# Kernel optimization log

Hardware: AMD Instinct MI355X
Metric: run time of the kernel (lower is better)

Reference implementation:

```python
import jax, jax.numpy as jnp
import numpy as np

M_POS = 0.5
M_NEG_SIM = 0.1
LAM_NEG = 1.0


def setup_inputs() -> dict:
    key = jax.random.key(0)
    N, d, G = 8192, 1024, 64
    codebook = jax.random.normal(key, (N, d), dtype=jnp.float32)
    base = (jnp.arange(N) // G) * G  # contiguous groups of size G (vq_to_range)
    starts = base.astype(jnp.int32)
    ends = (base + G - 1).astype(jnp.int32)
    return {"codebook": codebook, "starts": starts, "ends": ends, "max_i": N - 1}


def reference(codebook, starts, ends, max_i):
    N, d = codebook.shape
    M = min(N, int(max_i) + 1)  # rows processed by the python loop

    # cosine similarity rows [0:M] vs all N
    zn = codebook / jnp.linalg.norm(codebook, axis=-1, keepdims=True)
    cos = jnp.einsum('md,nd->mn', zn[:M], zn)  # (M, N)

    # pairwise Euclidean distances rows [0:M] vs all N via ||a-b||^2 = |a|^2+|b|^2-2ab
    sq = jnp.sum(codebook * codebook, axis=-1)  # (N,)
    dot = jnp.einsum('md,nd->mn', codebook[:M], codebook)  # (M, N)
    d2 = jnp.maximum(sq[:M, None] + sq[None, :] - 2.0 * dot, 0.0)

    j = jnp.arange(N)[None, :]
    i = jnp.arange(M)[:, None]
    in_range = (j >= starts[:M, None]) & (j <= ends[:M, None])
    pos_mask = in_range & (j != i)
    # original: group_mask[i]=False then neg = ~group_mask, so i is in negatives
    neg_mask = (~in_range) | (j == i)

    pos_cnt = jnp.sum(pos_mask, axis=-1)
    neg_cnt = jnp.sum(neg_mask, axis=-1)

    # safe sqrt: only evaluate on positive-mask entries
    D = jnp.sqrt(jnp.where(pos_mask, d2, 1.0))
    pos_term = jnp.square(jax.nn.relu(D - M_POS)) * pos_mask
    pos_pull = jnp.sum(pos_term, axis=-1) / jnp.maximum(pos_cnt, 1)

    neg_cos = jnp.clip(cos, -1.0, 1.0)
    neg_term = jnp.square(jax.nn.relu(jnp.abs(neg_cos) - M_NEG_SIM)) * neg_mask
    ortho = jnp.sum(neg_term, axis=-1) / jnp.maximum(neg_cnt, 1)

    valid = (pos_cnt > 0) & (neg_cnt > 0)
    per_row = jnp.where(valid, pos_pull + LAM_NEG * ortho, 0.0)
    cnt = jnp.sum(valid)
    total = jnp.sum(per_row)
    return jnp.where(cnt > 0, total / jnp.maximum(cnt, 1).astype(total.dtype), jnp.zeros((), total.dtype))
```

## Files before the change

### kernel.cpp

```cpp
#include <hip/hip_runtime.h>
#include <hip/hip_bf16.h>
#include <stdint.h>

#define M_POS 0.5f
#define M_NEG 0.1f
#define LAM_NEG 1.0f

typedef __attribute__((ext_vector_type(4))) float floatx4;
using f8x8 = long;

__global__ __launch_bounds__(256) void prep_kernel(
    const float* __restrict__ cb, unsigned char* __restrict__ cb_q,
    float* __restrict__ sq, float* __restrict__ inv_norm,
    unsigned* __restrict__ zero_base, int zero_len,
    int N, int d)
{
    const int gi = blockIdx.x * 256 + threadIdx.x;
    if (gi < zero_len) zero_base[gi] = 0u;

    const int row = blockIdx.x;
    const float* src = cb + (size_t)row * d;
    unsigned char* dst = cb_q + (size_t)row * d;
    const int t = threadIdx.x;

    float s = 0.f;
    for (int c = t * 4; c < d; c += 1024) {
        float4 v = *(const float4*)(src + c);
        s += v.x * v.x + v.y * v.y + v.z * v.z + v.w * v.w;
        int pk = __builtin_amdgcn_cvt_pk_fp8_f32(v.x, v.y, 0, false);
        pk     = __builtin_amdgcn_cvt_pk_fp8_f32(v.z, v.w, pk, true);
        *(int*)(dst + c) = pk;
    }
    for (int o = 32; o > 0; o >>= 1) s += __shfl_down(s, o, 64);
    __shared__ float wsum[4];
    if ((t & 63) == 0) wsum[t >> 6] = s;
    __syncthreads();
    if (t == 0) {
        float tot = wsum[0] + wsum[1] + wsum[2] + wsum[3];
        sq[row] = tot;
        inv_norm[row] = rsqrtf(tot);
    }
}

__global__ __launch_bounds__(256, 3) void gram_loss_kernel(
    const unsigned char* __restrict__ A,
    const float* __restrict__ sq, const float* __restrict__ inv_norm,
    const int* __restrict__ starts, const int* __restrict__ ends,
    const int* __restrict__ max_ip,
    float* __restrict__ pos_acc, float* __restrict__ neg_acc,
    unsigned* __restrict__ counter, float* __restrict__ out,
    int N, int d)
{
    const int M = min(N, max_ip[0] + 1);

    const int t = blockIdx.x;
    int bx = (int)((sqrtf(8.f * (float)t + 1.f) - 1.f) * 0.5f);
    while ((bx + 1) * (bx + 2) / 2 <= t) bx++;
    while (bx * (bx + 1) / 2 > t) bx--;
    const int by = t - bx * (bx + 1) / 2;

    const int rowBase = by * 128;
    const int colBase = bx * 128;
    const bool isDiag = (by == bx);

    __shared__ alignas(16) unsigned char ldsA[128 * 128];
    __shared__ alignas(16) unsigned char ldsB[128 * 128];

    const int tid  = threadIdx.x;
    const int wave = tid >> 6;
    const int lane = tid & 63;
    const int wr = (wave >> 1) * 64;
    const int wc = (wave & 1) * 64;

    floatx4 acc[4][4];
#pragma unroll
    for (int a = 0; a < 4; ++a)
#pragma unroll
        for (int b = 0; b < 4; ++b) acc[a][b] = (floatx4){0.f, 0.f, 0.f, 0.f};

    const int sRow = lane >> 3;
    const int sChk = lane & 7;
    const int srcOffC = ((sChk ^ sRow) * 16);
    const int kTiles = d / 128;

    const int rl = lane & 15;
    const int g  = lane >> 4;
    const int fragOddB = (g & 1) * 8;
    const int fragChkBase = g >> 1;
    const int rx = rl & 7;

    for (int kt = 0; kt < kTiles; ++kt) {
        __syncthreads();
        const int k0 = kt * 128;
#pragma unroll
        for (int h = 0; h < 4; ++h) {
            const int r = wave * 32 + h * 8 + sRow;
            const unsigned char* ga = A + (size_t)(rowBase + r) * d + k0 + srcOffC;
            const unsigned char* gb = A + (size_t)(colBase + r) * d + k0 + srcOffC;
            __builtin_amdgcn_global_load_lds(
                (const __attribute__((address_space(1))) void*)ga,
                (__attribute__((address_space(3))) void*)(ldsA + r * 128 + sChk * 16), 16, 0, 0);
            __builtin_amdgcn_global_load_lds(
                (const __attribute__((address_space(1))) void*)gb,
                (__attribute__((address_space(3))) void*)(ldsB + r * 128 + sChk * 16), 16, 0, 0);
        }
        __syncthreads();

#pragma unroll
        for (int ko = 0; ko < 4; ++ko) {
            const int koff = ((2 * ko + fragChkBase) ^ rx) * 16 + fragOddB;
            f8x8 af[4], bf[4];
#pragma unroll
            for (int t4 = 0; t4 < 4; ++t4) {
                const int ra = wr + t4 * 16 + rl;
                const int rb = wc + t4 * 16 + rl;
                af[t4] = *(const f8x8*)(ldsA + ra * 128 + koff);
                bf[t4] = *(const f8x8*)(ldsB + rb * 128 + koff);
            }
#pragma unroll
            for (int rt = 0; rt < 4; ++rt)
#pragma unroll
                for (int ct = 0; ct < 4; ++ct)
                    acc[rt][ct] = __builtin_amdgcn_mfma_f32_16x16x32_fp8_fp8(
                        af[rt], bf[ct], acc[rt][ct], 0, 0, 0);
        }
    }

    const int q  = lane >> 4;
    const int jlo = colBase + wc;
    const int ilo = rowBase + wr;

    int   jn[4];
    float jinv[4];
    bool  jvalid[4];
#pragma unroll
    for (int ct = 0; ct < 4; ++ct) {
        const int j = jlo + ct * 16 + rl;
        jn[ct]  = j;
        jinv[ct] = inv_norm[j];
        jvalid[ct] = (j < M);
    }

    bool posLane = false;
    {
        const int ri = ilo + lane;
        if (ri < M) posLane |= (ends[ri] >= jlo) && (starts[ri] <= jlo + 63);
        if (!isDiag) {
            const int cj = jlo + lane;
            if (cj < M) posLane |= (ends[cj] >= ilo) && (starts[cj] <= ilo + 63);
        }
    }
    const bool fullPath = (__ballot(posLane) != 0ULL);

    float posc[4] = {0.f, 0.f, 0.f, 0.f};
    float negc[4] = {0.f, 0.f, 0.f, 0.f};

    if (fullPath) {
        int   jns[4], jne[4];
        float jsq[4];
#pragma unroll
        for (int ct = 0; ct < 4; ++ct) {
            jsq[ct] = sq[jn[ct]];
            jns[ct] = jvalid[ct] ? starts[jn[ct]] : 0;
            jne[ct] = jvalid[ct] ? ends[jn[ct]]   : -1;
        }
#pragma unroll
        for (int rt = 0; rt < 4; ++rt) {
            const int ibase = ilo + rt * 16 + q * 4;
#pragma unroll
            for (int reg = 0; reg < 4; ++reg) {
                const int i = ibase + reg;
                const bool rowValid = (i < M);
                const int ns = rowValid ? starts[i] : 0;
                const int ne = rowValid ? ends[i]   : -1;
                const float iinv = inv_norm[i];
                const float isq  = sq[i];
                float posp = 0.f, negp = 0.f;
#pragma unroll
                for (int ct = 0; ct < 4; ++ct) {
                    const float dot = acc[rt][ct][reg];
                    const int j = jn[ct];
                    float cosv = dot * iinv * jinv[ct];
                    cosv = fminf(fmaxf(cosv, -1.f), 1.f);
                    float tn = fmaxf(fabsf(cosv) - M_NEG, 0.f);
                    const float nterm = tn * tn;
                    const float d2 = fmaxf(isq + jsq[ct] - 2.f * dot, 0.f);
                    float tp = fmaxf(sqrtf(d2) - M_POS, 0.f);
                    const float pterm = tp * tp;
                    const bool dg = (j == i);
                    if (rowValid) {
                        const bool in_r = (j >= ns) && (j <= ne);
                        if (in_r && !dg) posp += pterm;
                        if (!in_r || dg) negp += nterm;
                    }
                    if (!isDiag && jvalid[ct]) {
                        const bool in_c = (i >= jns[ct]) && (i <= jne[ct]);
                        if (in_c && !dg) posc[ct] += pterm;
                        if (!in_c || dg) negc[ct] += nterm;
                    }
                }
#pragma unroll
                for (int m = 1; m < 16; m <<= 1) {
                    posp += __shfl_xor(posp, m, 64);
                    negp += __shfl_xor(negp, m, 64);
                }
                if (rowValid && rl == 0) {
                    atomicAdd(&pos_acc[i], posp);
                    atomicAdd(&neg_acc[i], negp);
                }
            }
        }
        if (!isDiag) {
#pragma unroll
            for (int ct = 0; ct < 4; ++ct) {
                posc[ct] += __shfl_xor(posc[ct], 16, 64);
                posc[ct] += __shfl_xor(posc[ct], 32, 64);
                negc[ct] += __shfl_xor(negc[ct], 16, 64);
                negc[ct] += __shfl_xor(negc[ct], 32, 64);
            }
            if (q == 0) {
#pragma unroll
                for (int ct = 0; ct < 4; ++ct) {
                    if (jvalid[ct]) {
                        atomicAdd(&pos_acc[jn[ct]], posc[ct]);
                        atomicAdd(&neg_acc[jn[ct]], negc[ct]);
                    }
                }
            }
        }
    } else {
#pragma unroll
        for (int rt = 0; rt < 4; ++rt) {
            const int ibase = ilo + rt * 16 + q * 4;
#pragma unroll
            for (int reg = 0; reg < 4; ++reg) {
                const int i = ibase + reg;
                const float iinv = inv_norm[i];
                float negp = 0.f;
#pragma unroll
                for (int ct = 0; ct < 4; ++ct) {
                    const float dot = acc[rt][ct][reg];
                    float cosv = dot * iinv * jinv[ct];
                    cosv = fminf(fmaxf(cosv, -1.f), 1.f);
                    float tn = fmaxf(fabsf(cosv) - M_NEG, 0.f);
                    const float nterm = tn * tn;
                    negp += nterm;
                    negc[ct] += nterm;
                }
#pragma unroll
                for (int m = 1; m < 16; m <<= 1)
                    negp += __shfl_xor(negp, m, 64);
                if ((i < M) && rl == 0)
                    atomicAdd(&neg_acc[i], negp);
            }
        }
        if (!isDiag) {
#pragma unroll
            for (int ct = 0; ct < 4; ++ct) {
                negc[ct] += __shfl_xor(negc[ct], 16, 64);
                negc[ct] += __shfl_xor(negc[ct], 32, 64);
            }
            if (q == 0) {
#pragma unroll
                for (int ct = 0; ct < 4; ++ct)
                    if (jvalid[ct])
                        atomicAdd(&neg_acc[jn[ct]], negc[ct]);
            }
        }
    }

    __shared__ bool amLast;
    __syncthreads();
    if (tid == 0) {
        __threadfence();
        unsigned old = atomicAdd(counter, 1u);
        amLast = (old == (unsigned)(gridDim.x - 1));
    }
    __syncthreads();
    if (amLast) {
        __threadfence();
        float total = 0.f;
        int cnt = 0;
        for (int i = tid; i < M; i += 256) {
            const float pa = __hip_atomic_load(&pos_acc[i], __ATOMIC_RELAXED, __HIP_MEMORY_SCOPE_AGENT);
            const float na = __hip_atomic_load(&neg_acc[i], __ATOMIC_RELAXED, __HIP_MEMORY_SCOPE_AGENT);
            const int ns = starts[i], ne = ends[i];
            const int lo = max(ns, 0), hi = min(ne, N - 1);
            const int inr = max(hi - lo + 1, 0);
            const bool dg = (i >= ns) && (i <= ne);
            const int pos_cnt = inr - (dg ? 1 : 0);
            const int neg_cnt = N - inr + (dg ? 1 : 0);
            if (pos_cnt > 0 && neg_cnt > 0) {
                total += pa / (float)max(pos_cnt, 1)
                       + LAM_NEG * na / (float)max(neg_cnt, 1);
                cnt++;
            }
        }
        for (int o = 32; o > 0; o >>= 1) {
            total += __shfl_down(total, o, 64);
            cnt   += __shfl_down(cnt, o, 64);
        }
        __shared__ float fin_ts[4];
        __shared__ int   fin_cs[4];
        if ((tid & 63) == 0) { fin_ts[tid >> 6] = total; fin_cs[tid >> 6] = cnt; }
        __syncthreads();
        if (tid == 0) {
            float T = fin_ts[0] + fin_ts[1] + fin_ts[2] + fin_ts[3];
            int   C = fin_cs[0] + fin_cs[1] + fin_cs[2] + fin_cs[3];
            out[0] = (C > 0) ? T / (float)C : 0.f;
        }
    }
}

extern "C" void kernel_launch(void* const* d_in, const int* in_sizes, int n_in,
                              void* d_out, int out_size, void* d_ws, size_t ws_size,
                              hipStream_t stream) {
    const float* cb     = (const float*)d_in[0];
    const int*   starts = (const int*)d_in[1];
    const int*   ends   = (const int*)d_in[2];
    const int*   max_ip = (const int*)d_in[3];
    float* out = (float*)d_out;

    const int N = in_sizes[1];
    const int d = in_sizes[0] / N;

    char* ws = (char*)d_ws;
    unsigned char* cb_q = (unsigned char*)ws;
    size_t off = ((size_t)N * d + 255) & ~(size_t)255;
    float* sq       = (float*)(ws + off); off += (size_t)N * 4;
    float* inv_norm = (float*)(ws + off); off += (size_t)N * 4;
    float* pos_acc  = (float*)(ws + off); off += (size_t)N * 4;
    float* neg_acc  = (float*)(ws + off); off += (size_t)N * 4;
    unsigned* counter = (unsigned*)(ws + off); off += 256;

    prep_kernel<<<N, 256, 0, stream>>>(cb, cb_q, sq, inv_norm,
                                       (unsigned*)pos_acc, 2 * N + 1, N, d);

    const int nb = N / 128;
    const int nBlocks = nb * (nb + 1) / 2;
    gram_loss_kernel<<<nBlocks, 256, 0, stream>>>(cb_q, sq, inv_norm, starts, ends,
                                                  max_ip, pos_acc, neg_acc, counter,
                                                  out, N, d);
}
```

Before: 213.0 us.

## Double-buffer LDS staging with 64-wide K tiles to overlap loads and MFMA

```diff
diff --git a/kernel.cpp b/kernel.cpp
--- a/kernel.cpp
+++ b/kernel.cpp
@@ -63,8 +63,7 @@
     const int colBase = bx * 128;
     const bool isDiag = (by == bx);
 
-    __shared__ alignas(16) unsigned char ldsA[128 * 128];
-    __shared__ alignas(16) unsigned char ldsB[128 * 128];
+    __shared__ alignas(16) unsigned char lds[2][2][128 * 64];
 
     const int tid  = threadIdx.x;
     const int wave = tid >> 6;
@@ -78,44 +77,53 @@
 #pragma unroll
         for (int b = 0; b < 4; ++b) acc[a][b] = (floatx4){0.f, 0.f, 0.f, 0.f};
 
-    const int sRow = lane >> 3;
-    const int sChk = lane & 7;
-    const int srcOffC = ((sChk ^ sRow) * 16);
-    const int kTiles = d / 128;
+    const int sR = lane >> 2;
+    const int sQ = lane & 3;
+    const int kTiles = d / 64;
 
     const int rl = lane & 15;
     const int g  = lane >> 4;
-    const int fragOddB = (g & 1) * 8;
-    const int fragChkBase = g >> 1;
-    const int rx = rl & 7;
-
-    for (int kt = 0; kt < kTiles; ++kt) {
-        __syncthreads();
-        const int k0 = kt * 128;
-#pragma unroll
-        for (int h = 0; h < 4; ++h) {
-            const int r = wave * 32 + h * 8 + sRow;
-            const unsigned char* ga = A + (size_t)(rowBase + r) * d + k0 + srcOffC;
-            const unsigned char* gb = A + (size_t)(colBase + r) * d + k0 + srcOffC;
+    const int rowx = (rl >> 1) & 3;
+    const int ghalf = g >> 1;
+    const int godd  = (g & 1) * 8;
+
+    auto stage = [&](int kt, int buf) {
+        const int k0 = kt * 64;
+#pragma unroll
+        for (int h = 0; h < 2; ++h) {
+            const int r = wave * 32 + h * 16 + sR;
+            const int srcQ = sQ ^ ((r >> 1) & 3);
+            const unsigned char* ga = A + (size_t)(rowBase + r) * d + k0 + srcQ * 16;
+            const unsigned char* gb = A + (size_t)(colBase + r) * d + k0 + srcQ * 16;
             __builtin_amdgcn_global_load_lds(
                 (const __attribute__((address_space(1))) void*)ga,
-                (__attribute__((address_space(3))) void*)(ldsA + r * 128 + sChk * 16), 16, 0, 0);
+                (__attribute__((address_space(3))) void*)(&lds[buf][0][0] + r * 64 + sQ * 16), 16, 0, 0);
             __builtin_amdgcn_global_load_lds(
                 (const __attribute__((address_space(1))) void*)gb,
-                (__attribute__((address_space(3))) void*)(ldsB + r * 128 + sChk * 16), 16, 0, 0);
-        }
+                (__attribute__((address_space(3))) void*)(&lds[buf][1][0] + r * 64 + sQ * 16), 16, 0, 0);
+        }
+    };
+
+    stage(0, 0);
+
+    for (int kt = 0; kt < kTiles; ++kt) {
+        const int cur = kt & 1;
         __syncthreads();
-
-#pragma unroll
-        for (int ko = 0; ko < 4; ++ko) {
-            const int koff = ((2 * ko + fragChkBase) ^ rx) * 16 + fragOddB;
+        if (kt + 1 < kTiles) stage(kt + 1, cur ^ 1);
+
+        const unsigned char* ldsA = &lds[cur][0][0];
+        const unsigned char* ldsB = &lds[cur][1][0];
+#pragma unroll
+        for (int ko = 0; ko < 2; ++ko) {
+            const int phys16 = ((ko * 2 + ghalf) ^ rowx);
+            const int koff = phys16 * 16 + godd;
             f8x8 af[4], bf[4];
 #pragma unroll
             for (int t4 = 0; t4 < 4; ++t4) {
                 const int ra = wr + t4 * 16 + rl;
                 const int rb = wc + t4 * 16 + rl;
-                af[t4] = *(const f8x8*)(ldsA + ra * 128 + koff);
-                bf[t4] = *(const f8x8*)(ldsB + rb * 128 + koff);
+                af[t4] = *(const f8x8*)(ldsA + ra * 64 + koff);
+                bf[t4] = *(const f8x8*)(ldsB + rb * 64 + koff);
             }
 #pragma unroll
             for (int rt = 0; rt < 4; ++rt)
```

Result: slower. 221.9 us (+4.2%).
